# Optimization experiments

Hardware: AMD Instinct MI355X
Metric: run time of the kernel (lower is better)

## Reference

```python
import jax, jax.numpy as jnp
import numpy as np

H, KVH, D, HID = 32, 8, 128, 4096
ROPE_LEN, THETA = 8192, 10000.0
MASK_OUT, MIN_REMAIN = 0.9, 128


def _rope_tables(dtype):
    inv_freq = 1.0 / (THETA ** (jnp.arange(0, D, 2, dtype=jnp.float32) / D))
    freqs = jnp.arange(ROPE_LEN, dtype=jnp.float32)[:, None] * inv_freq[None, :]
    emb = jnp.concatenate([freqs, freqs], axis=-1)  # [8192, 128]
    return jnp.cos(emb).astype(dtype), jnp.sin(emb).astype(dtype)


def _rotate_half(x):
    x1, x2 = x[..., : D // 2], x[..., D // 2:]
    return jnp.concatenate([-x2, x1], axis=-1)


def _apply_rope(x, pos, cos, sin):
    c, s = cos[pos][None, None], sin[pos][None, None]  # [1,1,L,D]
    return x * c + _rotate_half(x) * s


def setup_inputs() -> dict:
    key = jax.random.key(0)
    ks = jax.random.split(key, 11)
    S = 4096
    f = jnp.float32
    return {
        "hidden_states": jax.random.normal(ks[0], (1, 1, HID), f),
        "key_cache": jax.random.normal(ks[1], (1, H, S, D), f),
        "val_cache": jax.random.normal(ks[2], (1, H, S, D), f),
        "Wq": jax.random.normal(ks[3], (HID, HID), f) * 0.02,
        "Wk": jax.random.normal(ks[4], (HID, KVH * D), f) * 0.02,
        "Wv": jax.random.normal(ks[5], (HID, KVH * D), f) * 0.02,
        "Wo": jax.random.normal(ks[6], (HID, HID), f) * 0.02,
        "hash_proj1": jax.random.normal(ks[7], (1, H, D, D), f) * 0.001,
        "hash_bias1": jnp.zeros((1, H, 1, D), f),
        "hash_proj2": jax.random.normal(ks[8], (1, H, D, D), f) * 0.001,
        "hash_bias2": jnp.zeros((1, H, 1, D), f),
    }


def reference(hidden_states, key_cache, val_cache, Wq, Wk, Wv, Wo,
              hash_proj1, hash_bias1, hash_proj2, hash_bias2):
    B, Q, _ = hidden_states.shape  # B=1, Q=1 (decode step)
    G = H // KVH
    dtype = hidden_states.dtype

    # projections -> [B, heads, Q, D]
    ques = (hidden_states @ Wq).reshape(B, Q, H, D).transpose(0, 2, 1, 3)
    k_new = (hidden_states @ Wk).reshape(B, Q, KVH, D).transpose(0, 2, 1, 3)
    v_new = (hidden_states @ Wv).reshape(B, Q, KVH, D).transpose(0, 2, 1, 3)
    k_new = jnp.repeat(k_new, G, axis=1)  # repeat_kv
    v_new = jnp.repeat(v_new, G, axis=1)

    keys = jnp.concatenate([key_cache, k_new], axis=2)  # [1,H,K,D]
    vals = jnp.concatenate([val_cache, v_new], axis=2)
    K = keys.shape[2]

    cos, sin = _rope_tables(dtype)
    q_pos = K - Q + jnp.arange(Q)
    k_pos = jnp.arange(K)
    q_r = _apply_rope(ques, q_pos, cos, sin)
    k_r = _apply_rope(keys, k_pos, cos, sin)

    # per-head hash MLP: silu layer with residue, then linear layer with residue
    def hash_fn(x):
        h = jax.nn.silu(jnp.einsum('bhld,bhde->bhle', x, hash_proj1) + hash_bias1) + x
        h = (jnp.einsum('bhld,bhde->bhle', h, hash_proj2) + hash_bias2) + h
        return h

    q_hash = jnp.sign(hash_fn(q_r))
    k_hash = jnp.sign(hash_fn(k_r))
    draft_score = jnp.einsum('bhqd,bhkd->bhqk', q_hash, k_hash)  # LSH similarity

    num_remain = max(min(K, MIN_REMAIN), K - int(K * MASK_OUT))
    _, idx = jax.lax.top_k(draft_score, num_remain)  # [B,H,Q,num_remain]

    neg = jnp.finfo(dtype).min
    mask = jnp.full((B, H, Q, K), neg, dtype=dtype)
    bi = jnp.arange(B)[:, None, None, None]
    hi = jnp.arange(H)[None, :, None, None]
    qi = jnp.arange(Q)[None, None, :, None]
    mask = mask.at[bi, hi, qi, idx].set(0.0)

    scores = jnp.einsum('bhqd,bhkd->bhqk', q_r, k_r) / np.sqrt(D) + mask
    attn = jax.nn.softmax(scores, axis=-1)
    out = jnp.einsum('bhqk,bhkd->bhqd', attn, vals)
    out = out.transpose(0, 2, 1, 3).reshape(B, Q, HID) @ Wo
    return out
```

## Files before the change

kernel.cpp:

```cpp
#include <hip/hip_runtime.h>
#include <math.h>

#define NH 32
#define NKVH 8
#define HD 128

typedef _Float16 half8 __attribute__((ext_vector_type(8)));
typedef float f32x4 __attribute__((ext_vector_type(4)));

#define OFF_QPROJ 0
#define OFF_KNEW  4096
#define OFF_VNEW  5120
#define OFF_QR    6144
#define OFF_QHASH 10240
#define OFF_TAB   10368

__global__ void init_kernel(const float* __restrict__ hp1, const float* __restrict__ hp2,
                            float* __restrict__ ws, float* __restrict__ out,
                            int K, int nInit) {
    const int tid = threadIdx.x;
    if ((int)blockIdx.x < nInit) {
        int idx = blockIdx.x * 256 + tid;
        if (idx < K * 64) {
            int pos = idx >> 6, d = idx & 63;
            double inv = exp(-((double)d / 64.0) * log(10000.0));
            double ang = (double)pos * inv;
            double s, c;
            sincos(ang, &s, &c);
            ws[OFF_TAB + idx]                  = (float)c;
            ws[OFF_TAB + (size_t)K * 64 + idx] = (float)s;
        }
        if (idx < 6144) ws[OFF_QPROJ + idx] = 0.f;
        if (idx < 4096) out[idx] = 0.f;
        size_t off_attn = OFF_TAB + 2 * (size_t)K * 64 + 2 * (size_t)NH * K;
        if (idx < 4096) ws[off_attn + idx] = 0.f;
    } else {
        int id = blockIdx.x - nInit;
        int h2 = id >> 3;
        int tg = (id & 7) * 256 + tid;
        const int lane = tg & 63, nt = (tg >> 6) & 7, ks = tg >> 9;
        const int kbase = ks * 32 + ((tg >> 4) & 3) * 8;
        const int n = nt * 16 + (tg & 15);
        const float* P = ((h2 & 1) ? hp2 : hp1) + (size_t)(h2 >> 1) * 16384;
        half8 v;
#pragma unroll
        for (int j = 0; j < 8; ++j) v[j] = (_Float16)P[(size_t)(kbase + j) * 128 + n];
        size_t off_pt = OFF_TAB + 2 * (size_t)K * 64 + 2 * (size_t)NH * K + 4096 + 2 * (size_t)NH * 512;
        ((half8*)(ws + off_pt))[(size_t)h2 * 2048 + tg] = v;
    }
}

__global__ __launch_bounds__(256) void qkv_gemv(const float* __restrict__ hidden,
        const float* __restrict__ Wq, const float* __restrict__ Wk,
        const float* __restrict__ Wv, float* __restrict__ ws) {
    __shared__ float hs[32];
    const int tid = threadIdx.x;
    const int col = (blockIdx.x * 256 + tid) * 4;
    const int i0  = blockIdx.y * 32;
    if (tid < 32) hs[tid] = hidden[i0 + tid];
    __syncthreads();
    const float* W; int ld, wcol;
    if (col < 4096)      { W = Wq; ld = 4096; wcol = col; }
    else if (col < 5120) { W = Wk; ld = 1024; wcol = col - 4096; }
    else                 { W = Wv; ld = 1024; wcol = col - 5120; }
    const float* p = W + (size_t)i0 * ld + wcol;
    float4 a0 = {0.f,0.f,0.f,0.f}, a1 = {0.f,0.f,0.f,0.f};
#pragma unroll 4
    for (int ii = 0; ii < 32; ii += 2) {
        float4 w0 = *(const float4*)p;
        float4 w1 = *(const float4*)(p + ld);
        float h0 = hs[ii], h1 = hs[ii + 1];
        a0.x = fmaf(h0, w0.x, a0.x); a0.y = fmaf(h0, w0.y, a0.y);
        a0.z = fmaf(h0, w0.z, a0.z); a0.w = fmaf(h0, w0.w, a0.w);
        a1.x = fmaf(h1, w1.x, a1.x); a1.y = fmaf(h1, w1.y, a1.y);
        a1.z = fmaf(h1, w1.z, a1.z); a1.w = fmaf(h1, w1.w, a1.w);
        p += 2 * (size_t)ld;
    }
    atomicAdd(&ws[OFF_QPROJ + col + 0], a0.x + a1.x);
    atomicAdd(&ws[OFF_QPROJ + col + 1], a0.y + a1.y);
    atomicAdd(&ws[OFF_QPROJ + col + 2], a0.z + a1.z);
    atomicAdd(&ws[OFF_QPROJ + col + 3], a0.w + a1.w);
}

__global__ __launch_bounds__(128) void qhash_kernel(const float* __restrict__ hp1,
        const float* __restrict__ hb1, const float* __restrict__ hp2,
        const float* __restrict__ hb2, float* __restrict__ ws, int S) {
    const int h = blockIdx.x, d = threadIdx.x;
    const int K = S + 1;
    __shared__ float X[128], H1[128];
    float q  = ws[OFF_QPROJ + h * 128 + d];
    float qp = ws[OFF_QPROJ + h * 128 + (d ^ 64)];
    const float* cosT = ws + OFF_TAB;
    const float* sinT = cosT + (size_t)K * 64;
    float cs = cosT[(size_t)S * 64 + (d & 63)];
    float sn = sinT[(size_t)S * 64 + (d & 63)];
    float r = (d < 64) ? -qp : qp;
    float qr = q * cs + r * sn;
    X[d] = qr;
    ws[OFF_QR + h * 128 + d] = qr;
    __syncthreads();
    const float* P1 = hp1 + (size_t)h * 16384;
    float t = hb1[h * 128 + d];
    for (int i = 0; i < 128; ++i) t = fmaf(X[i], P1[i * 128 + d], t);
    float u = t / (1.f + expf(-t)) + X[d];
    H1[d] = u;
    __syncthreads();
    const float* P2 = hp2 + (size_t)h * 16384;
    float t2 = hb2[h * 128 + d] + u;
    for (int i = 0; i < 128; ++i) t2 = fmaf(H1[i], P2[i * 128 + d], t2);
    unsigned long long bal = __ballot(t2 > 0.f);
    if ((d & 63) == 0)
        ((unsigned long long*)(ws + OFF_QHASH))[h * 2 + (d >> 6)] = bal;
}

__global__ __launch_bounds__(256, 4) void key_kernel(const float* __restrict__ key_cache,
        const float* __restrict__ hb1, const float* __restrict__ hb2,
        float* __restrict__ ws, int S) {
    const int K  = S + 1;
    const int h  = blockIdx.y;
    const int k0 = blockIdx.x * 64;
    const int tid = threadIdx.x;
    const int wv = tid >> 6, lane = tid & 63;
    const int m = lane & 15, quad = lane >> 4;

    __shared__ float XF[64 * 132];

    const float* cosT = ws + OFF_TAB;
    const float* sinT = cosT + (size_t)K * 64;
    float* scores = ws + OFF_TAB + 2 * (size_t)K * 64;
    int*   draft  = (int*)(scores + (size_t)NH * K);
    size_t off_pt = OFF_TAB + 2 * (size_t)K * 64 + 2 * (size_t)NH * K + 4096 + 2 * (size_t)NH * 512;
    const half8* PT1 = (const half8*)((const _Float16*)(ws + off_pt) + (size_t)(h * 2) * 16384);
    const half8* PT2 = PT1 + 2048;

    const int row = wv * 16 + m;
    const int kg  = k0 + row;
    const int cbase = quad * 8;
    float xr[4][8];
    if (kg < K) {
        const float* krow = (kg < S) ? key_cache + ((size_t)h * S + kg) * 128
                                     : ws + OFF_KNEW + (h >> 2) * 128;
        float xv[4][8];
#pragma unroll
        for (int c = 0; c < 4; ++c) {
            *(float4*)&xv[c][0] = *(const float4*)(krow + c * 32 + cbase);
            *(float4*)&xv[c][4] = *(const float4*)(krow + c * 32 + cbase + 4);
        }
        float cc[2][8], ss[2][8];
#pragma unroll
        for (int c = 0; c < 2; ++c) {
            *(float4*)&cc[c][0] = *(const float4*)(cosT + (size_t)kg * 64 + c * 32 + cbase);
            *(float4*)&cc[c][4] = *(const float4*)(cosT + (size_t)kg * 64 + c * 32 + cbase + 4);
            *(float4*)&ss[c][0] = *(const float4*)(sinT + (size_t)kg * 64 + c * 32 + cbase);
            *(float4*)&ss[c][4] = *(const float4*)(sinT + (size_t)kg * 64 + c * 32 + cbase + 4);
        }
#pragma unroll
        for (int c = 0; c < 2; ++c)
#pragma unroll
            for (int j = 0; j < 8; ++j) {
                xr[c][j]     = xv[c][j]     * cc[c][j] - xv[c + 2][j] * ss[c][j];
                xr[c + 2][j] = xv[c + 2][j] * cc[c][j] + xv[c][j]     * ss[c][j];
            }
    } else {
#pragma unroll
        for (int c = 0; c < 4; ++c)
#pragma unroll
            for (int j = 0; j < 8; ++j) xr[c][j] = 0.f;
    }

#pragma unroll
    for (int c = 0; c < 4; ++c) {
        *(float4*)&XF[row * 132 + c * 32 + cbase]     = *(float4*)&xr[c][0];
        *(float4*)&XF[row * 132 + c * 32 + cbase + 4] = *(float4*)&xr[c][4];
    }

    {
        const float* qr = ws + OFF_QR + h * 128;
        float part = 0.f;
#pragma unroll
        for (int c = 0; c < 4; ++c) {
            float4 qa = *(const float4*)(qr + c * 32 + cbase);
            float4 qb = *(const float4*)(qr + c * 32 + cbase + 4);
            part = fmaf(qa.x, xr[c][0], part); part = fmaf(qa.y, xr[c][1], part);
            part = fmaf(qa.z, xr[c][2], part); part = fmaf(qa.w, xr[c][3], part);
            part = fmaf(qb.x, xr[c][4], part); part = fmaf(qb.y, xr[c][5], part);
            part = fmaf(qb.z, xr[c][6], part); part = fmaf(qb.w, xr[c][7], part);
        }
        part += __shfl_xor(part, 16);
        part += __shfl_xor(part, 32);
        if (quad == 0 && kg < K) scores[(size_t)h * K + kg] = part * 0.08838834764831845f;
    }

    half8 af[4];
#pragma unroll
    for (int c = 0; c < 4; ++c)
#pragma unroll
        for (int j = 0; j < 8; ++j) af[c][j] = (_Float16)xr[c][j];

    f32x4 acc[8];

#pragma unroll
    for (int nt = 0; nt < 8; ++nt) acc[nt] = (f32x4){0.f, 0.f, 0.f, 0.f};
#pragma unroll
    for (int c = 0; c < 4; ++c)
#pragma unroll
        for (int nt = 0; nt < 8; ++nt)
            acc[nt] = __builtin_amdgcn_mfma_f32_16x16x32_f16(af[c], PT1[c * 512 + nt * 64 + lane], acc[nt], 0, 0, 0);

#pragma unroll
    for (int nt = 0; nt < 8; ++nt) {
        const int n = nt * 16 + m;
        float b1v = hb1[h * 128 + n];
#pragma unroll
        for (int r = 0; r < 4; ++r) {
            const int kk = wv * 16 + quad * 4 + r;
            float t = acc[nt][r] + b1v;
            float x = XF[kk * 132 + n];
            float h1v = t / (1.f + expf(-t)) + x;
            XF[kk * 132 + n] = h1v;
        }
    }

#pragma unroll
    for (int nt = 0; nt < 8; ++nt) acc[nt] = (f32x4){0.f, 0.f, 0.f, 0.f};
#pragma unroll
    for (int c = 0; c < 4; ++c) {
        float4 f0 = *(const float4*)&XF[row * 132 + c * 32 + cbase];
        float4 f1 = *(const float4*)&XF[row * 132 + c * 32 + cbase + 4];
        half8 a2;
        a2[0] = (_Float16)f0.x; a2[1] = (_Float16)f0.y;
        a2[2] = (_Float16)f0.z; a2[3] = (_Float16)f0.w;
        a2[4] = (_Float16)f1.x; a2[5] = (_Float16)f1.y;
        a2[6] = (_Float16)f1.z; a2[7] = (_Float16)f1.w;
#pragma unroll
        for (int nt = 0; nt < 8; ++nt)
            acc[nt] = __builtin_amdgcn_mfma_f32_16x16x32_f16(a2, PT2[c * 512 + nt * 64 + lane], acc[nt], 0, 0, 0);
    }

    {
        unsigned short qh16[8];
        uint4 q4 = *(const uint4*)((const unsigned*)(ws + OFF_QHASH) + h * 4);
        unsigned qa[4] = {q4.x, q4.y, q4.z, q4.w};
#pragma unroll
        for (int nt = 0; nt < 8; ++nt)
            qh16[nt] = (unsigned short)((qa[nt >> 1] >> ((nt & 1) * 16)) & 0xFFFFu);

        int ham[4] = {0, 0, 0, 0};
#pragma unroll
        for (int nt = 0; nt < 8; ++nt) {
            const int n = nt * 16 + m;
            float b2v = hb2[h * 128 + n];
#pragma unroll
            for (int r = 0; r < 4; ++r) {
                const int kk = wv * 16 + quad * 4 + r;
                float t2 = acc[nt][r] + b2v + XF[kk * 132 + n];
                unsigned long long bal = __ballot(t2 > 0.f);
                unsigned bits = (unsigned)(bal >> (quad * 16)) & 0xFFFFu;
                ham[r] += __popc(bits ^ (unsigned)qh16[nt]);
            }
        }
        if (m == 0) {
#pragma unroll
            for (int r = 0; r < 4; ++r) {
                int kgd = k0 + wv * 16 + quad * 4 + r;
                if (kgd < K) draft[(size_t)h * K + kgd] = 128 - 2 * ham[r];
            }
        }
    }
}

__global__ __launch_bounds__(256) void select_kernel(float* __restrict__ ws, int S, int nrem) {
    const int K = S + 1;
    const int h = blockIdx.x;
    const int tid = threadIdx.x;
    __shared__ int hist[129];
    __shared__ int sel_idx[512];
    __shared__ float red[256];
    __shared__ int wtot[4];
    __shared__ int sh_tval, sh_r, sh_cnt, sh_run;

    float* scoresB = ws + OFF_TAB + 2 * (size_t)K * 64;
    const int* draft = (const int*)(scoresB + (size_t)NH * K) + (size_t)h * K;
    const float* sc = scoresB + (size_t)h * K;
    float* attn = scoresB + 2 * (size_t)NH * K;
    int*   selidx_g = (int*)(attn + 4096) + h * 512;
    float* selw_g   = (attn + 4096 + NH * 512) + h * 512;

    for (int i = tid; i < 129; i += 256) hist[i] = 0;
    if (tid == 0) { sh_cnt = 0; sh_run = 0; }
    __syncthreads();
    for (int k = tid; k < K; k += 256) atomicAdd(&hist[(draft[k] + 128) >> 1], 1);
    __syncthreads();
    if (tid == 0) {
        int cum = 0, tb = 0, r = nrem;
        for (int b = 128; b >= 0; --b) {
            int c = hist[b];
            if (cum + c >= nrem) { tb = b; r = nrem - cum; break; }
            cum += c;
        }
        sh_tval = tb * 2 - 128; sh_r = r;
    }
    __syncthreads();
    const int tval = sh_tval, r = sh_r;
    const int lane = tid & 63, wave = tid >> 6;
    for (int base = 0; base < K; base += 256) {
        int k = base + tid;
        bool valid = (k < K);
        int dv = valid ? draft[k] : -1000;
        bool eq = valid && (dv == tval);
        bool gt = valid && (dv > tval);
        unsigned long long bal = __ballot(eq);
        if (lane == 0) wtot[wave] = __popcll(bal);
        __syncthreads();
        int woff = 0;
        for (int w = 0; w < wave; ++w) woff += wtot[w];
        int rank = sh_run + woff + __popcll(bal & ((1ull << lane) - 1ull));
        bool sel = gt || (eq && (rank < r));
        if (sel) sel_idx[atomicAdd(&sh_cnt, 1)] = k;
        __syncthreads();
        if (tid == 0) sh_run += wtot[0] + wtot[1] + wtot[2] + wtot[3];
        __syncthreads();
    }
    float mmax = -3.402823466e38f;
    for (int li = tid; li < nrem; li += 256) mmax = fmaxf(mmax, sc[sel_idx[li]]);
    red[tid] = mmax; __syncthreads();
    for (int s2 = 128; s2 > 0; s2 >>= 1) {
        if (tid < s2) red[tid] = fmaxf(red[tid], red[tid + s2]);
        __syncthreads();
    }
    mmax = red[0]; __syncthreads();
    float z = 0.f;
    for (int li = tid; li < nrem; li += 256) z += expf(sc[sel_idx[li]] - mmax);
    red[tid] = z; __syncthreads();
    for (int s2 = 128; s2 > 0; s2 >>= 1) {
        if (tid < s2) red[tid] += red[tid + s2];
        __syncthreads();
    }
    float Z = red[0]; __syncthreads();
    for (int li = tid; li < nrem; li += 256) {
        int idx = sel_idx[li];
        selidx_g[li] = idx;
        selw_g[li] = expf(sc[idx] - mmax) / Z;
    }
}

__global__ __launch_bounds__(256) void gather_kernel(const float* __restrict__ val_cache,
        float* __restrict__ ws, int S, int nrem) {
    const int K = S + 1;
    const int h = blockIdx.x, g = blockIdx.y;
    const int tid = threadIdx.x;
    const int wave = tid >> 6, lane = tid & 63;
    const int stream = g * 4 + wave;
    float* scoresB = ws + OFF_TAB + 2 * (size_t)K * 64;
    float* attn = scoresB + 2 * (size_t)NH * K;
    const int*   selidx_g = (const int*)(attn + 4096) + h * 512;
    const float* selw_g   = (attn + 4096 + NH * 512) + h * 512;
    float ax = 0.f, ay = 0.f;
    for (int li = stream; li < nrem; li += 128) {
        int idx = selidx_g[li];
        float w = selw_g[li];
        const float* vr = (idx < S) ? val_cache + ((size_t)h * S + idx) * 128
                                    : ws + OFF_VNEW + (h >> 2) * 128;
        float2 v = ((const float2*)vr)[lane];
        ax = fmaf(w, v.x, ax);
        ay = fmaf(w, v.y, ay);
    }
    atomicAdd(&attn[h * 128 + lane * 2 + 0], ax);
    atomicAdd(&attn[h * 128 + lane * 2 + 1], ay);
}

__global__ __launch_bounds__(256) void out_gemv(const float* __restrict__ Wo,
        const float* __restrict__ ws, float* __restrict__ out, int K) {
    __shared__ float hs[32];
    const int tid = threadIdx.x;
    const int col = (blockIdx.x * 256 + tid) * 4;
    const int i0  = blockIdx.y * 32;
    const float* ao = ws + OFF_TAB + 2 * (size_t)K * 64 + 2 * (size_t)NH * K;
    if (tid < 32) hs[tid] = ao[i0 + tid];
    __syncthreads();
    const float* p = Wo + (size_t)i0 * 4096 + col;
    float4 a0 = {0.f,0.f,0.f,0.f}, a1 = {0.f,0.f,0.f,0.f};
#pragma unroll 4
    for (int ii = 0; ii < 32; ii += 2) {
        float4 w0 = *(const float4*)p;
        float4 w1 = *(const float4*)(p + 4096);
        float h0 = hs[ii], h1 = hs[ii + 1];
        a0.x = fmaf(h0, w0.x, a0.x); a0.y = fmaf(h0, w0.y, a0.y);
        a0.z = fmaf(h0, w0.z, a0.z); a0.w = fmaf(h0, w0.w, a0.w);
        a1.x = fmaf(h1, w1.x, a1.x); a1.y = fmaf(h1, w1.y, a1.y);
        a1.z = fmaf(h1, w1.z, a1.z); a1.w = fmaf(h1, w1.w, a1.w);
        p += 8192;
    }
    atomicAdd(&out[col + 0], a0.x + a1.x);
    atomicAdd(&out[col + 1], a0.y + a1.y);
    atomicAdd(&out[col + 2], a0.z + a1.z);
    atomicAdd(&out[col + 3], a0.w + a1.w);
}

extern "C" void kernel_launch(void* const* d_in, const int* in_sizes, int n_in,
                              void* d_out, int out_size, void* d_ws, size_t ws_size,
                              hipStream_t stream) {
    const float* hidden = (const float*)d_in[0];
    const float* key_cache = (const float*)d_in[1];
    const float* val_cache = (const float*)d_in[2];
    const float* Wq = (const float*)d_in[3];
    const float* Wk = (const float*)d_in[4];
    const float* Wv = (const float*)d_in[5];
    const float* Wo = (const float*)d_in[6];
    const float* hp1 = (const float*)d_in[7];
    const float* hb1 = (const float*)d_in[8];
    const float* hp2 = (const float*)d_in[9];
    const float* hb2 = (const float*)d_in[10];
    float* out = (float*)d_out;
    float* ws  = (float*)d_ws;

    const int S = in_sizes[1] / (NH * HD);
    const int K = S + 1;
    int mn = (K < 128) ? K : 128;
    int nrem = K - (int)((double)K * 0.9);
    if (nrem < mn) nrem = mn;

    const int nInit = (K * 64 + 255) / 256;
    init_kernel<<<nInit + 512, 256, 0, stream>>>(hp1, hp2, ws, out, K, nInit);
    qkv_gemv<<<dim3(6, 128), 256, 0, stream>>>(hidden, Wq, Wk, Wv, ws);
    qhash_kernel<<<NH, 128, 0, stream>>>(hp1, hb1, hp2, hb2, ws, S);
    key_kernel<<<dim3((K + 63) / 64, NH), 256, 0, stream>>>(key_cache, hb1, hb2, ws, S);
    select_kernel<<<NH, 256, 0, stream>>>(ws, S, nrem);
    gather_kernel<<<dim3(NH, 32), 256, 0, stream>>>(val_cache, ws, S, nrem);
    out_gemv<<<dim3(4, 128), 256, 0, stream>>>(Wo, ws, out, K);
}
```

Baseline: 359.6 us.

## Swizzle key-kernel shared memory, hoist bias/hash loads, and halve GEMV/gather grids

In key_kernel the padded 132-stride shared tile becomes an unpadded 128-stride tile with an XOR swizzle to avoid bank conflicts. Hash bias and query-hash loads are hoisted ahead of the RoPE compute, and the occupancy hint moves to amdgpu_waves_per_eu. Separately, the QKV and output GEMVs each process 64 rows per block instead of 32, halving the grid and the atomicAdd count. The gather kernel also uses half as many blocks, each doing more iterations. Larger per-block work lowers atomic and launch overhead but reduces parallelism for memory-bound GEMVs.

```diff
diff --git a/kernel.cpp b/kernel.cpp
--- a/kernel.cpp
+++ b/kernel.cpp
@@ -53,11 +53,11 @@
 __global__ __launch_bounds__(256) void qkv_gemv(const float* __restrict__ hidden,
         const float* __restrict__ Wq, const float* __restrict__ Wk,
         const float* __restrict__ Wv, float* __restrict__ ws) {
-    __shared__ float hs[32];
+    __shared__ float hs[64];
     const int tid = threadIdx.x;
     const int col = (blockIdx.x * 256 + tid) * 4;
-    const int i0  = blockIdx.y * 32;
-    if (tid < 32) hs[tid] = hidden[i0 + tid];
+    const int i0  = blockIdx.y * 64;
+    if (tid < 64) hs[tid] = hidden[i0 + tid];
     __syncthreads();
     const float* W; int ld, wcol;
     if (col < 4096)      { W = Wq; ld = 4096; wcol = col; }
@@ -66,7 +66,7 @@
     const float* p = W + (size_t)i0 * ld + wcol;
     float4 a0 = {0.f,0.f,0.f,0.f}, a1 = {0.f,0.f,0.f,0.f};
 #pragma unroll 4
-    for (int ii = 0; ii < 32; ii += 2) {
+    for (int ii = 0; ii < 64; ii += 2) {
         float4 w0 = *(const float4*)p;
         float4 w1 = *(const float4*)(p + ld);
         float h0 = hs[ii], h1 = hs[ii + 1];
@@ -113,7 +113,8 @@
         ((unsigned long long*)(ws + OFF_QHASH))[h * 2 + (d >> 6)] = bal;
 }
 
-__global__ __launch_bounds__(256, 4) void key_kernel(const float* __restrict__ key_cache,
+__global__ __launch_bounds__(256) __attribute__((amdgpu_waves_per_eu(4, 5)))
+void key_kernel(const float* __restrict__ key_cache,
         const float* __restrict__ hb1, const float* __restrict__ hb2,
         float* __restrict__ ws, int S) {
     const int K  = S + 1;
@@ -122,8 +123,11 @@
     const int tid = threadIdx.x;
     const int wv = tid >> 6, lane = tid & 63;
     const int m = lane & 15, quad = lane >> 4;
-
-    __shared__ float XF[64 * 132];
+    const int row = wv * 16 + m;
+    const int cbase = quad * 8;
+    const int sw = (m & 7) << 2;
+
+    __shared__ float XF[64 * 128];
 
     const float* cosT = ws + OFF_TAB;
     const float* sinT = cosT + (size_t)K * 64;
@@ -133,19 +137,40 @@
     const half8* PT1 = (const half8*)((const _Float16*)(ws + off_pt) + (size_t)(h * 2) * 16384);
     const half8* PT2 = PT1 + 2048;
 
-    const int row = wv * 16 + m;
-    const int kg  = k0 + row;
-    const int cbase = quad * 8;
+    const int kg = k0 + row;
+
     float xr[4][8];
     if (kg < K) {
         const float* krow = (kg < S) ? key_cache + ((size_t)h * S + kg) * 128
                                      : ws + OFF_KNEW + (h >> 2) * 128;
-        float xv[4][8];
 #pragma unroll
         for (int c = 0; c < 4; ++c) {
-            *(float4*)&xv[c][0] = *(const float4*)(krow + c * 32 + cbase);
-            *(float4*)&xv[c][4] = *(const float4*)(krow + c * 32 + cbase + 4);
-        }
+            *(float4*)&xr[c][0] = *(const float4*)(krow + c * 32 + cbase);
+            *(float4*)&xr[c][4] = *(const float4*)(krow + c * 32 + cbase + 4);
+        }
+    } else {
+#pragma unroll
+        for (int c = 0; c < 4; ++c)
+#pragma unroll
+            for (int j = 0; j < 8; ++j) xr[c][j] = 0.f;
+    }
+
+    float b1v[8], b2v[8];
+#pragma unroll
+    for (int nt = 0; nt < 8; ++nt) {
+        b1v[nt] = hb1[h * 128 + nt * 16 + m];
+        b2v[nt] = hb2[h * 128 + nt * 16 + m];
+    }
+    unsigned short qh16[8];
+    {
+        uint4 q4 = *(const uint4*)((const unsigned*)(ws + OFF_QHASH) + h * 4);
+        unsigned qa[4] = {q4.x, q4.y, q4.z, q4.w};
+#pragma unroll
+        for (int nt = 0; nt < 8; ++nt)
+            qh16[nt] = (unsigned short)((qa[nt >> 1] >> ((nt & 1) * 16)) & 0xFFFFu);
+    }
+
+    if (kg < K) {
         float cc[2][8], ss[2][8];
 #pragma unroll
         for (int c = 0; c < 2; ++c) {
@@ -158,20 +183,16 @@
         for (int c = 0; c < 2; ++c)
 #pragma unroll
             for (int j = 0; j < 8; ++j) {
-                xr[c][j]     = xv[c][j]     * cc[c][j] - xv[c + 2][j] * ss[c][j];
-                xr[c + 2][j] = xv[c + 2][j] * cc[c][j] + xv[c][j]     * ss[c][j];
+                float lo = xr[c][j]     * cc[c][j] - xr[c + 2][j] * ss[c][j];
+                float hi = xr[c + 2][j] * cc[c][j] + xr[c][j]     * ss[c][j];
+                xr[c][j] = lo; xr[c + 2][j] = hi;
             }
-    } else {
-#pragma unroll
-        for (int c = 0; c < 4; ++c)
-#pragma unroll
-            for (int j = 0; j < 8; ++j) xr[c][j] = 0.f;
     }
 
 #pragma unroll
     for (int c = 0; c < 4; ++c) {
-        *(float4*)&XF[row * 132 + c * 32 + cbase]     = *(float4*)&xr[c][0];
-        *(float4*)&XF[row * 132 + c * 32 + cbase + 4] = *(float4*)&xr[c][4];
+        *(float4*)&XF[row * 128 + ((c * 32 + cbase) ^ sw)]     = *(float4*)&xr[c][0];
+        *(float4*)&XF[row * 128 + ((c * 32 + cbase + 4) ^ sw)] = *(float4*)&xr[c][4];
     }
 
     {
@@ -210,14 +231,13 @@
 #pragma unroll
     for (int nt = 0; nt < 8; ++nt) {
         const int n = nt * 16 + m;
-        float b1v = hb1[h * 128 + n];
 #pragma unroll
         for (int r = 0; r < 4; ++r) {
             const int kk = wv * 16 + quad * 4 + r;
-            float t = acc[nt][r] + b1v;
-            float x = XF[kk * 132 + n];
-            float h1v = t / (1.f + expf(-t)) + x;
-            XF[kk * 132 + n] = h1v;
+            const int nn = n ^ ((kk & 7) << 2);
+            float t = acc[nt][r] + b1v[nt];
+            float x = XF[kk * 128 + nn];
+            XF[kk * 128 + nn] = t / (1.f + expf(-t)) + x;
         }
     }
 
@@ -225,8 +245,8 @@
     for (int nt = 0; nt < 8; ++nt) acc[nt] = (f32x4){0.f, 0.f, 0.f, 0.f};
 #pragma unroll
     for (int c = 0; c < 4; ++c) {
-        float4 f0 = *(const float4*)&XF[row * 132 + c * 32 + cbase];
-        float4 f1 = *(const float4*)&XF[row * 132 + c * 32 + cbase + 4];
+        float4 f0 = *(const float4*)&XF[row * 128 + ((c * 32 + cbase) ^ sw)];
+        float4 f1 = *(const float4*)&XF[row * 128 + ((c * 32 + cbase + 4) ^ sw)];
         half8 a2;
         a2[0] = (_Float16)f0.x; a2[1] = (_Float16)f0.y;
         a2[2] = (_Float16)f0.z; a2[3] = (_Float16)f0.w;
@@ -238,22 +258,14 @@
     }
 
     {
-        unsigned short qh16[8];
-        uint4 q4 = *(const uint4*)((const unsigned*)(ws + OFF_QHASH) + h * 4);
-        unsigned qa[4] = {q4.x, q4.y, q4.z, q4.w};
-#pragma unroll
-        for (int nt = 0; nt < 8; ++nt)
-            qh16[nt] = (unsigned short)((qa[nt >> 1] >> ((nt & 1) * 16)) & 0xFFFFu);
-
         int ham[4] = {0, 0, 0, 0};
 #pragma unroll
         for (int nt = 0; nt < 8; ++nt) {
             const int n = nt * 16 + m;
-            float b2v = hb2[h * 128 + n];
 #pragma unroll
             for (int r = 0; r < 4; ++r) {
                 const int kk = wv * 16 + quad * 4 + r;
-                float t2 = acc[nt][r] + b2v + XF[kk * 132 + n];
+                float t2 = acc[nt][r] + b2v[nt] + XF[kk * 128 + (n ^ ((kk & 7) << 2))];
                 unsigned long long bal = __ballot(t2 > 0.f);
                 unsigned bits = (unsigned)(bal >> (quad * 16)) & 0xFFFFu;
                 ham[r] += __popc(bits ^ (unsigned)qh16[nt]);
@@ -356,7 +368,7 @@
     const int*   selidx_g = (const int*)(attn + 4096) + h * 512;
     const float* selw_g   = (attn + 4096 + NH * 512) + h * 512;
     float ax = 0.f, ay = 0.f;
-    for (int li = stream; li < nrem; li += 128) {
+    for (int li = stream; li < nrem; li += 64) {
         int idx = selidx_g[li];
         float w = selw_g[li];
         const float* vr = (idx < S) ? val_cache + ((size_t)h * S + idx) * 128
@@ -371,17 +383,17 @@
 
 __global__ __launch_bounds__(256) void out_gemv(const float* __restrict__ Wo,
         const float* __restrict__ ws, float* __restrict__ out, int K) {
-    __shared__ float hs[32];
+    __shared__ float hs[64];
     const int tid = threadIdx.x;
     const int col = (blockIdx.x * 256 + tid) * 4;
-    const int i0  = blockIdx.y * 32;
+    const int i0  = blockIdx.y * 64;
     const float* ao = ws + OFF_TAB + 2 * (size_t)K * 64 + 2 * (size_t)NH * K;
-    if (tid < 32) hs[tid] = ao[i0 + tid];
+    if (tid < 64) hs[tid] = ao[i0 + tid];
     __syncthreads();
     const float* p = Wo + (size_t)i0 * 4096 + col;
     float4 a0 = {0.f,0.f,0.f,0.f}, a1 = {0.f,0.f,0.f,0.f};
 #pragma unroll 4
-    for (int ii = 0; ii < 32; ii += 2) {
+    for (int ii = 0; ii < 64; ii += 2) {
         float4 w0 = *(const float4*)p;
         float4 w1 = *(const float4*)(p + 4096);
         float h0 = hs[ii], h1 = hs[ii + 1];
@@ -422,10 +434,10 @@
 
     const int nInit = (K * 64 + 255) / 256;
     init_kernel<<<nInit + 512, 256, 0, stream>>>(hp1, hp2, ws, out, K, nInit);
-    qkv_gemv<<<dim3(6, 128), 256, 0, stream>>>(hidden, Wq, Wk, Wv, ws);
+    qkv_gemv<<<dim3(6, 64), 256, 0, stream>>>(hidden, Wq, Wk, Wv, ws);
     qhash_kernel<<<NH, 128, 0, stream>>>(hp1, hb1, hp2, hb2, ws, S);
     key_kernel<<<dim3((K + 63) / 64, NH), 256, 0, stream>>>(key_cache, hb1, hb2, ws, S);
     select_kernel<<<NH, 256, 0, stream>>>(ws, S, nrem);
-    gather_kernel<<<dim3(NH, 32), 256, 0, stream>>>(val_cache, ws, S, nrem);
-    out_gemv<<<dim3(4, 128), 256, 0, stream>>>(Wo, ws, out, K);
-}
+    gather_kernel<<<dim3(NH, 16), 256, 0, stream>>>(val_cache, ws, S, nrem);
+    out_gemv<<<dim3(4, 64), 256, 0, stream>>>(Wo, ws, out, K);
+}
```

Result: no change. 354.4 us (-1.4%).
